# Kernel tuning notes

Measured on AMD Instinct MI355X. Metric: run time of the kernel, lower is better.

The kernel has to match this reference:

```python
import jax, jax.numpy as jnp
import numpy as np

# ---- constants hard-coded in the torch module ----
NEG_EPS = 1e-30          # eps used in log clamps
TAU = 0.35               # near-field temperature (getattr default)
K0 = 128                 # near-field band width
C_EMBD, N_HEADS, RANK = 768, 12, 32
B, T = 1, 2048


def _lin(k, fin, fout):
    lim = 1.0 / np.sqrt(fin)
    return jax.random.uniform(k, (fin, fout), jnp.float32, -lim, lim)


def _bias(k, fin, fout):
    lim = 1.0 / np.sqrt(fin)
    return jax.random.uniform(k, (fout,), jnp.float32, -lim, lim)


def setup_inputs() -> dict:
    key = jax.random.key(0)
    ks = jax.random.split(key, 24)
    C, H, R = C_EMBD, N_HEADS, RANK
    return {
        "x": jax.random.normal(ks[0], (B, T, C), jnp.float32),
        "Wq_w": _lin(ks[1], C, C), "Wq_b": _bias(ks[2], C, C),
        "Wk_w": _lin(ks[3], C, C), "Wk_b": _bias(ks[4], C, C),
        "Wv_w": _lin(ks[5], C, C), "Wv_b": _bias(ks[6], C, C),
        "Wo_w": _lin(ks[7], C, C), "Wo_b": _bias(ks[8], C, C),
        "Pq_w": _lin(ks[9], C, R),
        "Pk_w": _lin(ks[10], C, R),
        "Pv_w": _lin(ks[11], C, R),
        "up_w": _lin(ks[12], R, C),
        "gate_u": jax.random.normal(ks[13], (H, C // H), jnp.float32),
        "gate_b": jnp.zeros((H,), jnp.float32),
        "Wz_w": _lin(ks[14], 4 * C, C), "Wz_b": _bias(ks[15], 4 * C, C),
    }


def reference(x, Wq_w, Wq_b, Wk_w, Wk_b, Wv_w, Wv_b, Wo_w, Wo_b,
              Pq_w, Pk_w, Pv_w, up_w, gate_u, gate_b, Wz_w, Wz_b):
    Bx, Tx, C = x.shape
    H = gate_u.shape[0]
    D = C // H
    R = Pq_w.shape[1]
    k0 = min(K0, Tx - 1)
    kernel = k0 + 1
    b_scalar = -np.log(max(Tx, 1)).astype(np.float32) if hasattr(np.log(1.0), 'astype') else -np.log(max(Tx, 1))
    b_scalar = jnp.float32(-np.log(max(Tx, 1)))

    # 0) projections + heads
    Q = x @ Wq_w + Wq_b
    K = x @ Wk_w + Wk_b
    V = x @ Wv_w + Wv_b
    heads = lambda z: z.reshape(Bx, Tx, H, D).transpose(0, 2, 1, 3)  # (B,H,T,D)
    Qh, Kh, Vh = heads(Q), heads(K), heads(V)

    idx = jnp.arange(Tx)
    causal = idx[None, :] <= idx[:, None]                  # (T,T)
    band = causal & ((idx[:, None] - idx[None, :]) <= k0)  # banded causal

    # 1) low-rank EA + sigmoid + LASER seed
    Qr, Kr, Vr = Q @ Pq_w, K @ Pk_w, V @ Pv_w              # (B,T,R)
    S = (Qr @ Kr.transpose(0, 2, 1)) * (1.0 / np.sqrt(R))  # (B,T,T)
    # masked logits were -1e9 -> sigmoid == 0 exactly in fp32
    A_seed = jnp.where(causal[None], jax.nn.sigmoid(S * S + b_scalar), 0.0)
    # running causal max over keys, per feature (== amax of causally masked keys)
    m_seed = jax.lax.cummax(Vr, axis=1)                    # (B,T,R)
    Yr = jnp.einsum('bij,bjr->bir', A_seed, jnp.exp(Vr)) * jnp.exp(-m_seed)
    H0 = (jnp.log(jnp.maximum(Yr, NEG_EPS)) + m_seed) @ up_w  # (B,T,C)

    # 2a) near-field banded causal attention (cos^2 / tau, sigmoid, LASER)
    l2n = lambda z: z / jnp.maximum(jnp.linalg.norm(z, axis=-1, keepdims=True), 1e-12)
    cos = jnp.einsum('bhid,bhjd->bhij', l2n(Qh), l2n(Kh))  # (B,H,T,T)
    A_near = jnp.where(band[None, None], jax.nn.sigmoid(cos * cos / TAU + b_scalar), 0.0)
    # sliding-window (width kernel, past-only) max of V per feature
    m_near = jax.lax.reduce_window(
        Vh, -jnp.inf, jax.lax.max,
        window_dimensions=(1, 1, kernel, 1), window_strides=(1, 1, 1, 1),
        padding=[(0, 0), (0, 0), (kernel - 1, 0), (0, 0)])   # (B,H,T,D)
    V_exp = jnp.exp(Vh - m_near)
    Y_near = jnp.einsum('bhij,bhjd->bhid', A_near, V_exp)
    H_near = jnp.log(jnp.maximum(Y_near, NEG_EPS)) + m_near

    # 2b) far-field hierarchical levels: source truncates mid-loop; the
    # accumulator H_far_total_h is initialized to zeros -> contributes zero.
    Ht_h = H_near                                          # (B,H,T,D)

    # 3) head-wise sigmoid gating
    g = jax.nn.sigmoid(jnp.einsum('bhtd,hd->bht', Ht_h, gate_u) + gate_b[None, :, None])
    Ht_h = Ht_h * g[..., None]
    Htilde = Ht_h.transpose(0, 2, 1, 3).reshape(Bx, Tx, C)

    # 4) GRU blend (Wz consumes 4*C features)
    z = jax.nn.sigmoid(jnp.concatenate([x, H0, Htilde, H0 * Htilde], axis=-1) @ Wz_w + Wz_b)
    H_out = (1.0 - z) * H0 + z * Htilde
    return H_out @ Wo_w + Wo_b
```

## Files before the change

kernel.cpp:

```cpp
#include <hip/hip_runtime.h>
#include <math.h>

static constexpr float B_SCALAR    = -7.6246189861593985f;
static constexpr float INV_TAU     = 2.8571428571428571f;
static constexpr float INV_SQRT_R  = 0.17677669529663687f;

typedef __attribute__((ext_vector_type(8))) short bf16x8;
typedef __attribute__((ext_vector_type(4))) float f32x4;

__device__ __forceinline__ unsigned short f2b(float f) {
    union { float f; unsigned int u; } v; v.f = f;
    unsigned int r = v.u + 0x7fffu + ((v.u >> 16) & 1u);
    return (unsigned short)(r >> 16);
}

typedef const __attribute__((address_space(1))) unsigned int* gp1_t;
typedef __attribute__((address_space(3))) unsigned int* lp3_t;
__device__ __forceinline__ void gload16(const unsigned short* g, unsigned short* l) {
    __builtin_amdgcn_global_load_lds((gp1_t)g, (lp3_t)l, 16, 0, 0);
}

__device__ __forceinline__ bf16x8 frag128(const unsigned short* base, int row, int elem) {
    int byte = (row * 128 + elem * 2) ^ ((row & 7) << 4);
    return *(const bf16x8*)((const char*)base + byte);
}
__device__ __forceinline__ bf16x8 frag384(const unsigned short* base, int row, int elem) {
    int byte = (row * 384 + elem * 2) ^ ((row & 7) << 4);
    return *(const bf16x8*)((const char*)base + byte);
}

template<int MODE, int KZ>
__global__ __launch_bounds__(256) void gemm_mfma(
    const unsigned short* __restrict__ A0, const unsigned short* __restrict__ A1,
    const unsigned short* __restrict__ A2, const unsigned short* __restrict__ A3,
    const unsigned short* __restrict__ Bt, const float* __restrict__ bias,
    float* __restrict__ outf, unsigned short* __restrict__ outb,
    float* __restrict__ pbuf, int K, int ldo)
{
    __shared__ unsigned short As[2][128*64];
    __shared__ unsigned short Bs[2][128*64];
    const int tid = threadIdx.x;
    const int lane = tid & 63, wid = tid >> 6;
    const int wr = wid >> 1, wc = wid & 1;
    const int fr = lane & 15, fq = lane >> 4;
    const int n0 = blockIdx.x * 128, m0 = blockIdx.y * 128;
    const int kz = blockIdx.z;
    const int kslice = K / KZ;
    const int kbase = kz * kslice;
    const int nt = kslice / 64;

    f32x4 acc[4][4];
#pragma unroll
    for (int mi = 0; mi < 4; ++mi)
#pragma unroll
        for (int ni = 0; ni < 4; ++ni) acc[mi][ni] = (f32x4){0.f, 0.f, 0.f, 0.f};

    auto stage = [&](int buf, int k0) {
        const unsigned short* Ap;
        int k0l, ldA;
        if (MODE == 1) {
            int p = k0 / 768;
            Ap = (p == 0) ? A0 : (p == 1) ? A1 : (p == 2) ? A2 : A3;
            k0l = k0 - p * 768; ldA = 768;
        } else { Ap = A0; k0l = k0; ldA = K; }
#pragma unroll
        for (int i = 0; i < 4; ++i) {
            int cb = i * 256 + wid * 64;
            int c  = cb + lane;
            int r = c >> 3;
            int col = ((c & 7) ^ (r & 7)) * 8;
            gload16(Ap + (size_t)(m0 + r) * ldA + k0l + col, &As[buf][cb * 8]);
            gload16(Bt + (size_t)(n0 + r) * K   + k0  + col, &Bs[buf][cb * 8]);
        }
    };

    stage(0, kbase);
    asm volatile("s_waitcnt vmcnt(0)" ::: "memory");
    __builtin_amdgcn_s_barrier();
    __builtin_amdgcn_sched_barrier(0);

    int cur = 0;
    for (int t = 0; t < nt; ++t) {
        if (t + 1 < nt) stage(cur ^ 1, kbase + (t + 1) * 64);
#pragma unroll
        for (int kk = 0; kk < 64; kk += 32) {
            bf16x8 af[4], bfr[4];
#pragma unroll
            for (int mi = 0; mi < 4; ++mi)
                af[mi] = frag128(As[cur], wr*64 + mi*16 + fr, kk + fq*8);
#pragma unroll
            for (int ni = 0; ni < 4; ++ni)
                bfr[ni] = frag128(Bs[cur], wc*64 + ni*16 + fr, kk + fq*8);
#pragma unroll
            for (int mi = 0; mi < 4; ++mi)
#pragma unroll
                for (int ni = 0; ni < 4; ++ni)
                    acc[mi][ni] = __builtin_amdgcn_mfma_f32_16x16x32_bf16(
                        af[mi], bfr[ni], acc[mi][ni], 0, 0, 0);
        }
        asm volatile("s_waitcnt vmcnt(0)" ::: "memory");
        __builtin_amdgcn_s_barrier();
        __builtin_amdgcn_sched_barrier(0);
        cur ^= 1;
    }
#pragma unroll
    for (int mi = 0; mi < 4; ++mi)
#pragma unroll
        for (int ni = 0; ni < 4; ++ni)
#pragma unroll
            for (int v = 0; v < 4; ++v) {
                int m = m0 + wr*64 + mi*16 + fq*4 + v;
                int n = n0 + wc*64 + ni*16 + fr;
                float val = acc[mi][ni][v];
                if (KZ > 1) {
                    pbuf[((size_t)kz * 2048 + m) * 768 + n] = val;
                } else {
                    float vv = val + bias[n];
                    outf[(size_t)m * ldo + n] = vv;
                    if (MODE == 0) outb[(size_t)m * ldo + n] = f2b(vv);
                }
            }
}

__global__ __launch_bounds__(256) void wz_combine(
    const float* __restrict__ pbuf, const float* __restrict__ bz,
    const float* __restrict__ h0, const float* __restrict__ htl,
    unsigned short* __restrict__ outb)
{
    int i = blockIdx.x * 256 + threadIdx.x;
    if (i >= 2048*768/4) return;
    float4 s = *(const float4*)&pbuf[i*4];
    float4 p1 = *(const float4*)&pbuf[1536*1024 + i*4];
    float4 p2 = *(const float4*)&pbuf[2*1536*1024 + i*4];
    float4 p3 = *(const float4*)&pbuf[3*1536*1024 + i*4];
    s.x += p1.x + p2.x + p3.x; s.y += p1.y + p2.y + p3.y;
    s.z += p1.z + p2.z + p3.z; s.w += p1.w + p2.w + p3.w;
    float4 b = *(const float4*)&bz[(i % 192) * 4];
    float4 a = *(const float4*)&h0[i*4];
    float4 t = *(const float4*)&htl[i*4];
    float z0 = 1.f/(1.f+expf(-(s.x+b.x))), z1 = 1.f/(1.f+expf(-(s.y+b.y)));
    float z2 = 1.f/(1.f+expf(-(s.z+b.z))), z3 = 1.f/(1.f+expf(-(s.w+b.w)));
    outb[i*4+0] = f2b((1.f-z0)*a.x + z0*t.x);
    outb[i*4+1] = f2b((1.f-z1)*a.y + z1*t.y);
    outb[i*4+2] = f2b((1.f-z2)*a.z + z2*t.z);
    outb[i*4+3] = f2b((1.f-z3)*a.w + z3*t.w);
}

__global__ __launch_bounds__(256) void wo_combine(
    const float* __restrict__ pbuf, const float* __restrict__ bo,
    float* __restrict__ out)
{
    int i = blockIdx.x * 256 + threadIdx.x;
    if (i >= 2048*768/4) return;
    float4 s = *(const float4*)&pbuf[i*4];
    float4 p1 = *(const float4*)&pbuf[1536*1024 + i*4];
    float4 b = *(const float4*)&bo[(i % 192) * 4];
    float4 o;
    o.x = s.x + p1.x + b.x; o.y = s.y + p1.y + b.y;
    o.z = s.z + p1.z + b.z; o.w = s.w + p1.w + b.w;
    *(float4*)&out[i*4] = o;
}

__global__ __launch_bounds__(256) void cvt_bf16(const float* __restrict__ in,
                                                unsigned short* __restrict__ out, int n4)
{
    int i = blockIdx.x * 256 + threadIdx.x;
    if (i < n4) {
        float4 v = *(const float4*)&in[i * 4];
        out[i*4+0] = f2b(v.x); out[i*4+1] = f2b(v.y);
        out[i*4+2] = f2b(v.z); out[i*4+3] = f2b(v.w);
    }
}

__global__ __launch_bounds__(256) void transpose_w(const float* __restrict__ w,
                                                   unsigned short* __restrict__ wt,
                                                   int K, int N)
{
    __shared__ float tile[32][33];
    int kb = blockIdx.x * 32, nb = blockIdx.y * 32;
    int tx = threadIdx.x & 31, ty = threadIdx.x >> 5;
#pragma unroll
    for (int s = 0; s < 32; s += 8)
        tile[ty + s][tx] = w[(size_t)(kb + ty + s) * N + nb + tx];
    __syncthreads();
#pragma unroll
    for (int s = 0; s < 32; s += 8)
        wt[(size_t)(nb + ty + s) * K + kb + tx] = f2b(tile[tx][ty + s]);
}

__global__ void concat_bias(const float* __restrict__ bq, const float* __restrict__ bk,
                            const float* __restrict__ bv, float* __restrict__ o)
{
    int n = blockIdx.x * 256 + threadIdx.x;
    if (n < 2304) o[n] = (n < 768) ? bq[n] : (n < 1536) ? bk[n - 768] : bv[n - 1536];
}

__global__ __launch_bounds__(256) void build_gru_inputs(
    const float* __restrict__ h0, const float* __restrict__ hn,
    unsigned short* __restrict__ h0b, unsigned short* __restrict__ htlb,
    unsigned short* __restrict__ prodb, int n4)
{
    int i = blockIdx.x * 256 + threadIdx.x;
    if (i < n4) {
        float4 a = *(const float4*)&h0[i * 4];
        float4 b = *(const float4*)&hn[i * 4];
        h0b[i*4+0] = f2b(a.x); h0b[i*4+1] = f2b(a.y); h0b[i*4+2] = f2b(a.z); h0b[i*4+3] = f2b(a.w);
        htlb[i*4+0] = f2b(b.x); htlb[i*4+1] = f2b(b.y); htlb[i*4+2] = f2b(b.z); htlb[i*4+3] = f2b(b.w);
        prodb[i*4+0] = f2b(a.x*b.x); prodb[i*4+1] = f2b(a.y*b.y);
        prodb[i*4+2] = f2b(a.z*b.z); prodb[i*4+3] = f2b(a.w*b.w);
    }
}

__global__ __launch_bounds__(256) void lowrank_mfma(
    const unsigned short* __restrict__ qkvb, const unsigned short* __restrict__ pT,
    float* __restrict__ pbuf)
{
    __shared__ unsigned short As[2][128*64];
    __shared__ unsigned short Bs[2][32*64];
    const int tid = threadIdx.x, lane = tid & 63, wid = tid >> 6;
    const int fr = lane & 15, fq = lane >> 4;
    const int m0 = blockIdx.x * 128;
    const int sel = blockIdx.y, kz = blockIdx.z;
    const int kbase = kz * 192;

    f32x4 acc[2][2];
#pragma unroll
    for (int mi = 0; mi < 2; ++mi)
#pragma unroll
        for (int ni = 0; ni < 2; ++ni) acc[mi][ni] = (f32x4){0.f,0.f,0.f,0.f};

    auto stage = [&](int buf, int k0) {
#pragma unroll
        for (int i = 0; i < 4; ++i) {
            int cb = i * 256 + wid * 64, c = cb + lane;
            int r = c >> 3, col = ((c & 7) ^ (r & 7)) * 8;
            gload16(qkvb + (size_t)(m0 + r) * 2304 + sel*768 + k0 + col, &As[buf][cb * 8]);
        }
        {
            int cb = wid * 64, c = cb + lane;
            int r = c >> 3, col = ((c & 7) ^ (r & 7)) * 8;
            gload16(pT + (size_t)sel * 32*768 + (size_t)r * 768 + k0 + col, &Bs[buf][cb * 8]);
        }
    };

    stage(0, kbase);
    asm volatile("s_waitcnt vmcnt(0)" ::: "memory");
    __builtin_amdgcn_s_barrier();
    __builtin_amdgcn_sched_barrier(0);

    int cur = 0;
    for (int t = 0; t < 3; ++t) {
        if (t + 1 < 3) stage(cur ^ 1, kbase + (t + 1) * 64);
#pragma unroll
        for (int kk = 0; kk < 64; kk += 32) {
            bf16x8 a[2], b[2];
#pragma unroll
            for (int mi = 0; mi < 2; ++mi)
                a[mi] = frag128(As[cur], wid*32 + mi*16 + fr, kk + fq*8);
#pragma unroll
            for (int ni = 0; ni < 2; ++ni)
                b[ni] = frag128(Bs[cur], ni*16 + fr, kk + fq*8);
#pragma unroll
            for (int mi = 0; mi < 2; ++mi)
#pragma unroll
                for (int ni = 0; ni < 2; ++ni)
                    acc[mi][ni] = __builtin_amdgcn_mfma_f32_16x16x32_bf16(
                        a[mi], b[ni], acc[mi][ni], 0, 0, 0);
        }
        asm volatile("s_waitcnt vmcnt(0)" ::: "memory");
        __builtin_amdgcn_s_barrier();
        __builtin_amdgcn_sched_barrier(0);
        cur ^= 1;
    }
#pragma unroll
    for (int mi = 0; mi < 2; ++mi)
#pragma unroll
        for (int ni = 0; ni < 2; ++ni)
#pragma unroll
            for (int v = 0; v < 4; ++v) {
                int m = m0 + wid*32 + mi*16 + fq*4 + v;
                int n = ni*16 + fr;
                pbuf[((size_t)(kz*3 + sel) * 2048 + m) * 32 + n] = acc[mi][ni][v];
            }
}

__global__ __launch_bounds__(256) void lowrank_finish(
    const float* __restrict__ pbuf,
    unsigned short* __restrict__ qrb, unsigned short* __restrict__ krb,
    float* __restrict__ vr, unsigned short* __restrict__ evtb)
{
    int idx = blockIdx.x * 256 + threadIdx.x;
    int sel = idx >> 16, rem = idx & 65535;
    float s = pbuf[(size_t)(0*3 + sel)*65536 + rem]
            + pbuf[(size_t)(1*3 + sel)*65536 + rem]
            + pbuf[(size_t)(2*3 + sel)*65536 + rem]
            + pbuf[(size_t)(3*3 + sel)*65536 + rem];
    if (sel == 0)      qrb[rem] = f2b(s * INV_SQRT_R);
    else if (sel == 1) krb[rem] = f2b(s);
    else {
        int t = rem >> 5, r = rem & 31;
        vr[rem] = s;
        evtb[(size_t)r * 2048 + t] = f2b(expf(s));
    }
}

__global__ __launch_bounds__(256) void cummax_vr(const float* __restrict__ vr,
                                                 float* __restrict__ ms)
{
    __shared__ float part[256];
    int r = blockIdx.x, tid = threadIdx.x;
    int t0 = tid * 8;
    float v[8];
    float run = -INFINITY;
#pragma unroll
    for (int e = 0; e < 8; ++e) { run = fmaxf(run, vr[(t0+e)*32 + r]); v[e] = run; }
    part[tid] = run;
    __syncthreads();
    for (int off = 1; off < 256; off <<= 1) {
        float other = (tid >= off) ? part[tid - off] : -INFINITY;
        __syncthreads();
        part[tid] = fmaxf(part[tid], other);
        __syncthreads();
    }
    float excl = (tid > 0) ? part[tid - 1] : -INFINITY;
#pragma unroll
    for (int e = 0; e < 8; ++e) ms[(t0+e)*32 + r] = fmaxf(v[e], excl);
}

__global__ __launch_bounds__(256) void seed_mfma(
    const unsigned short* __restrict__ qrb, const unsigned short* __restrict__ krb,
    const unsigned short* __restrict__ evtb, float* __restrict__ partial)
{
    int it = blockIdx.x, jc = blockIdx.y;
    if (jc > it) return;
    const int i0 = it * 128, j0 = jc * 128;
    __shared__ unsigned short Qs[128*32];
    __shared__ unsigned short Ks[128*32];
    __shared__ unsigned short Es[32*128];
    __shared__ unsigned short Ps[128*128];
    const int tid = threadIdx.x, lane = tid & 63, wid = tid >> 6;
    const int fr = lane & 15, fq = lane >> 4;

#pragma unroll
    for (int s = 0; s < 2; ++s) {
        int cb = s * 256 + wid * 64;
        int c = cb + lane;
        int r = c >> 2, col = (c & 3) * 8;
        gload16(qrb + (size_t)(i0 + r) * 32 + col, &Qs[cb * 8]);
        gload16(krb + (size_t)(j0 + r) * 32 + col, &Ks[cb * 8]);
    }
#pragma unroll
    for (int s = 0; s < 2; ++s) {
        int c = s * 256 + tid;
        int rr = c >> 4, cc = c & 15;
        bf16x8 v = *(const bf16x8*)&evtb[(size_t)rr * 2048 + j0 + cc * 8];
        int byte = (rr * 256 + cc * 16) ^ ((rr & 7) << 4);
        *(bf16x8*)((char*)Es + byte) = v;
    }
    __syncthreads();

    const int wr = wid >> 1, wc = wid & 1;
    bf16x8 af[4], bk[4];
#pragma unroll
    for (int mi = 0; mi < 4; ++mi)
        af[mi] = *(const bf16x8*)&Qs[(wr*64 + mi*16 + fr)*32 + fq*8];
#pragma unroll
    for (int ni = 0; ni < 4; ++ni)
        bk[ni] = *(const bf16x8*)&Ks[(wc*64 + ni*16 + fr)*32 + fq*8];
#pragma unroll
    for (int mi = 0; mi < 4; ++mi)
#pragma unroll
        for (int ni = 0; ni < 4; ++ni) {
            f32x4 s4 = __builtin_amdgcn_mfma_f32_16x16x32_bf16(
                af[mi], bk[ni], (f32x4){0.f,0.f,0.f,0.f}, 0, 0, 0);
#pragma unroll
            for (int v = 0; v < 4; ++v) {
                int row = wr*64 + mi*16 + fq*4 + v;
                int col = wc*64 + ni*16 + fr;
                float a = 0.f;
                if (j0 + col <= i0 + row) {
                    float s = s4[v];
                    a = 1.f / (1.f + expf(-(s*s + B_SCALAR)));
                }
                int byte = (row * 256 + col * 2) ^ ((row & 7) << 4);
                *(unsigned short*)((char*)Ps + byte) = f2b(a);
            }
        }
    __syncthreads();

    f32x4 yacc[2][2];
#pragma unroll
    for (int mi = 0; mi < 2; ++mi)
#pragma unroll
        for (int nf = 0; nf < 2; ++nf) yacc[mi][nf] = (f32x4){0.f,0.f,0.f,0.f};
#pragma unroll
    for (int ks = 0; ks < 4; ++ks) {
        bf16x8 pa[2], eb[2];
#pragma unroll
        for (int mi = 0; mi < 2; ++mi) {
            int row = wid*32 + mi*16 + fr;
            int byte = (row * 256 + ks * 64 + fq * 16) ^ ((row & 7) << 4);
            pa[mi] = *(const bf16x8*)((const char*)Ps + byte);
        }
#pragma unroll
        for (int nf = 0; nf < 2; ++nf) {
            int rrow = nf*16 + fr;
            int byte = (rrow * 256 + ks * 64 + fq * 16) ^ ((rrow & 7) << 4);
            eb[nf] = *(const bf16x8*)((const char*)Es + byte);
        }
#pragma unroll
        for (int mi = 0; mi < 2; ++mi)
#pragma unroll
            for (int nf = 0; nf < 2; ++nf)
                yacc[mi][nf] = __builtin_amdgcn_mfma_f32_16x16x32_bf16(
                    pa[mi], eb[nf], yacc[mi][nf], 0, 0, 0);
    }
    float* pout = partial + ((size_t)(it*16 + jc) * 128) * 32;
#pragma unroll
    for (int mi = 0; mi < 2; ++mi)
#pragma unroll
        for (int nf = 0; nf < 2; ++nf)
#pragma unroll
            for (int v = 0; v < 4; ++v) {
                int row = wid*32 + mi*16 + fq*4 + v;
                int col = nf*16 + fr;
                pout[row*32 + col] = yacc[mi][nf][v];
            }
}

__global__ __launch_bounds__(256) void seed_finish(const float* __restrict__ partial,
                                                   const float* __restrict__ ms,
                                                   float* __restrict__ lr)
{
    int idx = blockIdx.x * 256 + threadIdx.x;
    int i = idx >> 5, r = idx & 31;
    int it = i >> 7, row = i & 127;
    float y = 0.f;
    for (int jjc = 0; jjc <= it; ++jjc)
        y += partial[(((size_t)(it*16 + jjc) * 128) + row) * 32 + r];
    float m = ms[idx];
    lr[idx] = logf(fmaxf(y * expf(-m), 1e-30f)) + m;
}

__global__ __launch_bounds__(256) void up_proj(const float* __restrict__ lr,
                                               const float* __restrict__ up,
                                               float* __restrict__ h0)
{
    __shared__ float ls[32];
    int t = blockIdx.x, tid = threadIdx.x;
    if (tid < 32) ls[tid] = lr[t*32 + tid];
    __syncthreads();
    for (int c = tid; c < 768; c += 256) {
        float acc = 0.f;
#pragma unroll
        for (int rr = 0; rr < 32; ++rr) acc = fmaf(ls[rr], up[rr*768 + c], acc);
        h0[t*768 + c] = acc;
    }
}

__global__ void head_norms_write(const float* __restrict__ qkv,
                                 unsigned short* __restrict__ qhatb,
                                 unsigned short* __restrict__ khatb)
{
    int t = blockIdx.x, tid = threadIdx.x;
    int h = tid >> 6, d = tid & 63;
    float q = qkv[t*2304 + h*64 + d];
    float k = qkv[t*2304 + 768 + h*64 + d];
    float sq = q*q, sk = k*k;
#pragma unroll
    for (int off = 32; off; off >>= 1) { sq += __shfl_xor(sq, off); sk += __shfl_xor(sk, off); }
    float iq = 1.f / fmaxf(sqrtf(sq), 1e-12f);
    float ik = 1.f / fmaxf(sqrtf(sk), 1e-12f);
    qhatb[(size_t)t*768 + h*64 + d] = f2b(q * iq);
    khatb[(size_t)t*768 + h*64 + d] = f2b(k * ik);
}

__global__ __launch_bounds__(256) void slide_max(const float* __restrict__ qkv,
                                                 float* __restrict__ mnear,
                                                 unsigned short* __restrict__ vexptb)
{
    __shared__ float vs[192][64];
    int c0 = blockIdx.x * 64, t0 = blockIdx.y * 64;
    int tid = threadIdx.x;
#pragma unroll
    for (int s = 0; s < 12; ++s) {
        int idx = tid + s * 256;
        int rr = idx >> 4, c4 = (idx & 15) * 4;
        int t = t0 - 128 + rr;
        float4 v4;
        if (t < 0) v4 = make_float4(-INFINITY, -INFINITY, -INFINITY, -INFINITY);
        else       v4 = *(const float4*)&qkv[t*2304 + 1536 + c0 + c4];
        *(float4*)&vs[rr][c4] = v4;
    }
    __syncthreads();
    int c = tid & 63, tg = tid >> 6;
    for (int u = 0; u < 16; ++u) {
        int tl = tg * 16 + u;
        float m = -INFINITY;
        for (int s = 0; s < 129; ++s) m = fmaxf(m, vs[tl + s][c]);
        float v = vs[tl + 128][c];
        int t = t0 + tl;
        mnear[(size_t)t*768 + c0 + c] = m;
        vexptb[(size_t)(c0 + c) * 2048 + t] = f2b(expf(v - m));
    }
}

__global__ __launch_bounds__(256) void near_fused(
    const unsigned short* __restrict__ qhatb, const unsigned short* __restrict__ khatb,
    const unsigned short* __restrict__ vexptb, const float* __restrict__ mnear,
    const float* __restrict__ gu, const float* __restrict__ gb,
    float* __restrict__ hn)
{
    __shared__ unsigned short Qs[64*64];
    __shared__ unsigned short KPs[192*64];
    __shared__ unsigned short Vst[64*192];
    const int it = blockIdx.x, hh = blockIdx.y;
    const int i0 = it * 64;
    const int tid = threadIdx.x, lane = tid & 63, wid = tid >> 6;
    const int fr = lane & 15, fq = lane >> 4;

#pragma unroll
    for (int i = 0; i < 2; ++i) {
        int cb = i * 256 + wid * 64, c = cb + lane;
        int r = c >> 3, col = ((c & 7) ^ (r & 7)) * 8;
        gload16(qhatb + (size_t)(i0 + r) * 768 + hh*64 + col, &Qs[cb * 8]);
    }
#pragma unroll
    for (int i = 0; i < 6; ++i) {
        int cb = i * 256 + wid * 64, c = cb + lane;
        int r = c >> 3, col = ((c & 7) ^ (r & 7)) * 8;
        int j = i0 - 128 + r; if (j < 0) j = 0;
        gload16(khatb + (size_t)j * 768 + hh*64 + col, &KPs[cb * 8]);
    }
#pragma unroll
    for (int i = 0; i < 6; ++i) {
        int cb = i * 256 + wid * 64, c = cb + lane;
        int d = c / 24, cc = c - d * 24;
        int ccp = (cc & 24) | ((cc & 7) ^ (d & 7));
        int t = i0 - 128 + ccp * 8; if (t < 0) t = 0;
        gload16(vexptb + (size_t)(hh*64 + d) * 2048 + t, &Vst[cb * 8]);
    }
    __syncthreads();

    f32x4 sacc[4][3];
#pragma unroll
    for (int mi = 0; mi < 4; ++mi)
#pragma unroll
        for (int ni = 0; ni < 3; ++ni) sacc[mi][ni] = (f32x4){0.f,0.f,0.f,0.f};
#pragma unroll
    for (int kt = 0; kt < 2; ++kt) {
        int kk = kt * 32;
        bf16x8 qa[4], kb[3];
#pragma unroll
        for (int mi = 0; mi < 4; ++mi)
            qa[mi] = frag128(Qs, mi*16 + fr, kk + fq*8);
#pragma unroll
        for (int ni = 0; ni < 3; ++ni)
            kb[ni] = frag128(KPs, wid*48 + ni*16 + fr, kk + fq*8);
#pragma unroll
        for (int mi = 0; mi < 4; ++mi)
#pragma unroll
            for (int ni = 0; ni < 3; ++ni)
                sacc[mi][ni] = __builtin_amdgcn_mfma_f32_16x16x32_bf16(
                    qa[mi], kb[ni], sacc[mi][ni], 0, 0, 0);
    }
    __syncthreads();

#pragma unroll
    for (int mi = 0; mi < 4; ++mi)
#pragma unroll
        for (int ni = 0; ni < 3; ++ni)
#pragma unroll
            for (int v = 0; v < 4; ++v) {
                int il = mi*16 + fq*4 + v;
                int jl = wid*48 + ni*16 + fr;
                float s = sacc[mi][ni][v];
                float a = 0.f;
                if (jl >= il && jl <= il + 128 && (i0 - 128 + jl) >= 0)
                    a = 1.f / (1.f + expf(-(s*s*INV_TAU + B_SCALAR)));
                int byte = (il * 384 + jl * 2) ^ ((il & 7) << 4);
                *(unsigned short*)((char*)KPs + byte) = f2b(a);
            }
    __syncthreads();

    f32x4 yacc[4];
#pragma unroll
    for (int nf = 0; nf < 4; ++nf) yacc[nf] = (f32x4){0.f,0.f,0.f,0.f};
#pragma unroll
    for (int ks = 0; ks < 6; ++ks) {
        int kk = ks * 32;
        bf16x8 pa = frag384(KPs, wid*16 + fr, kk + fq*8);
        bf16x8 vb[4];
#pragma unroll
        for (int nf = 0; nf < 4; ++nf)
            vb[nf] = frag384(Vst, nf*16 + fr, kk + fq*8);
#pragma unroll
        for (int nf = 0; nf < 4; ++nf)
            yacc[nf] = __builtin_amdgcn_mfma_f32_16x16x32_bf16(pa, vb[nf], yacc[nf], 0, 0, 0);
    }

    float hv[4][4];
    float sp[4] = {0.f, 0.f, 0.f, 0.f};
#pragma unroll
    for (int nf = 0; nf < 4; ++nf) {
        int d = nf*16 + fr;
        float guv = gu[hh*64 + d];
#pragma unroll
        for (int v = 0; v < 4; ++v) {
            int row = wid*16 + fq*4 + v;
            float y = yacc[nf][v];
            float h = logf(fmaxf(y, 1e-30f)) + mnear[(size_t)(i0 + row)*768 + hh*64 + d];
            hv[nf][v] = h;
            sp[v] = fmaf(h, guv, sp[v]);
        }
    }
#pragma unroll
    for (int off = 1; off < 16; off <<= 1) {
#pragma unroll
        for (int v = 0; v < 4; ++v) sp[v] += __shfl_xor(sp[v], off);
    }
    float gbh = gb[hh];
#pragma unroll
    for (int v = 0; v < 4; ++v) sp[v] = 1.f / (1.f + expf(-(sp[v] + gbh)));
#pragma unroll
    for (int nf = 0; nf < 4; ++nf)
#pragma unroll
        for (int v = 0; v < 4; ++v) {
            int row = wid*16 + fq*4 + v;
            int d = nf*16 + fr;
            hn[(size_t)(i0 + row)*768 + hh*64 + d] = hv[nf][v] * sp[v];
        }
}

extern "C" void kernel_launch(void* const* d_in, const int* in_sizes, int n_in,
                              void* d_out, int out_size, void* d_ws, size_t ws_size,
                              hipStream_t stream)
{
    const float* x  = (const float*)d_in[0];
    const float* wq = (const float*)d_in[1];  const float* bq = (const float*)d_in[2];
    const float* wk = (const float*)d_in[3];  const float* bk = (const float*)d_in[4];
    const float* wv = (const float*)d_in[5];  const float* bv = (const float*)d_in[6];
    const float* wo = (const float*)d_in[7];  const float* bo = (const float*)d_in[8];
    const float* pq = (const float*)d_in[9];  const float* pk = (const float*)d_in[10];
    const float* pv = (const float*)d_in[11];
    const float* up = (const float*)d_in[12];
    const float* gu = (const float*)d_in[13]; const float* gb = (const float*)d_in[14];
    const float* wz = (const float*)d_in[15]; const float* bz = (const float*)d_in[16];
    float* out = (float*)d_out;

    float* w = (float*)d_ws;
    float* qkv  = w; w += 2048*2304;
    float* vr   = w; w += 2048*32;
    float* ms   = w; w += 2048*32;
    float* lr   = w; w += 2048*32;
    float* h0   = w; w += 2048*768;
    float* mnear= w; w += 2048*768;
    float* hn   = w; w += 2048*768;
    float* partial = w; w += 16*16*128*32;
    float* pgemm = w; w += 4*2048*768;
    float* plr   = w; w += 4*3*2048*32;
    float* bqkv = w; w += 2304;
    unsigned short* xb     = (unsigned short*)w; w += 2048*768/2;
    unsigned short* qkvb   = (unsigned short*)w; w += 2048*2304/2;
    unsigned short* wqkvT  = (unsigned short*)w; w += 2304*768/2;
    unsigned short* wzT    = (unsigned short*)w; w += 768*3072/2;
    unsigned short* woT    = (unsigned short*)w; w += 768*768/2;
    unsigned short* pT     = (unsigned short*)w; w += 3*32*768/2;
    unsigned short* h0b    = (unsigned short*)w; w += 2048*768/2;
    unsigned short* htlb   = (unsigned short*)w; w += 2048*768/2;
    unsigned short* prodb  = (unsigned short*)w; w += 2048*768/2;
    unsigned short* houtb  = (unsigned short*)w; w += 2048*768/2;
    unsigned short* qrb    = (unsigned short*)w; w += 2048*32/2;
    unsigned short* krb    = (unsigned short*)w; w += 2048*32/2;
    unsigned short* evtb   = (unsigned short*)w; w += 32*2048/2;
    unsigned short* qhatb  = (unsigned short*)w; w += 2048*768/2;
    unsigned short* khatb  = (unsigned short*)w; w += 2048*768/2;
    unsigned short* vexptb = (unsigned short*)w; w += 768*2048/2;

    cvt_bf16<<<1536, 256, 0, stream>>>(x, xb, 2048*768/4);
    transpose_w<<<dim3(24,24), 256, 0, stream>>>(wq, wqkvT,            768, 768);
    transpose_w<<<dim3(24,24), 256, 0, stream>>>(wk, wqkvT + 768*768,  768, 768);
    transpose_w<<<dim3(24,24), 256, 0, stream>>>(wv, wqkvT + 1536*768, 768, 768);
    transpose_w<<<dim3(96,24), 256, 0, stream>>>(wz, wzT, 3072, 768);
    transpose_w<<<dim3(24,24), 256, 0, stream>>>(wo, woT, 768, 768);
    transpose_w<<<dim3(24,1),  256, 0, stream>>>(pq, pT,            768, 32);
    transpose_w<<<dim3(24,1),  256, 0, stream>>>(pk, pT + 32*768,   768, 32);
    transpose_w<<<dim3(24,1),  256, 0, stream>>>(pv, pT + 2*32*768, 768, 32);
    concat_bias<<<9, 256, 0, stream>>>(bq, bk, bv, bqkv);

    gemm_mfma<0,1><<<dim3(18,16,1), 256, 0, stream>>>(xb, nullptr, nullptr, nullptr,
        wqkvT, bqkv, qkv, qkvb, nullptr, 768, 2304);

    lowrank_mfma<<<dim3(16,3,4), 256, 0, stream>>>(qkvb, pT, plr);
    lowrank_finish<<<768, 256, 0, stream>>>(plr, qrb, krb, vr, evtb);
    cummax_vr<<<32, 256, 0, stream>>>(vr, ms);
    seed_mfma<<<dim3(16,16), 256, 0, stream>>>(qrb, krb, evtb, partial);
    seed_finish<<<256, 256, 0, stream>>>(partial, ms, lr);
    up_proj<<<2048, 256, 0, stream>>>(lr, up, h0);

    head_norms_write<<<2048, 768, 0, stream>>>(qkv, qhatb, khatb);
    slide_max<<<dim3(12,32), 256, 0, stream>>>(qkv, mnear, vexptb);
    near_fused<<<dim3(32,12), 256, 0, stream>>>(qhatb, khatb, vexptb, mnear, gu, gb, hn);

    build_gru_inputs<<<1536, 256, 0, stream>>>(h0, hn, h0b, htlb, prodb, 2048*768/4);
    gemm_mfma<1,4><<<dim3(6,16,4), 256, 0, stream>>>(xb, h0b, htlb, prodb,
        wzT, nullptr, nullptr, nullptr, pgemm, 3072, 768);
    wz_combine<<<1536, 256, 0, stream>>>(pgemm, bz, h0, hn, houtb);
    gemm_mfma<2,2><<<dim3(6,16,2), 256, 0, stream>>>(houtb, nullptr, nullptr, nullptr,
        woT, nullptr, nullptr, nullptr, pgemm, 768, 768);
    wo_combine<<<1536, 256, 0, stream>>>(pgemm, bo, out);
}
```

Before: 180.9 us.

## Merge prep kernels, fuse seed/up-proj and GRU input casts, speed sliding max

The ten weight/input preparation launches are merged into one prep_all kernel that dispatches by block index. seed_finish is folded into up_proj, which now also writes the bf16 copy of h0. near_fused now writes the bf16 Htilde and H0*Htilde products, so the build_gru_inputs pass is gone. slide_max computes its 129-wide window max from a shared core range plus prefix and suffix maxima instead of a full scan per row. Together these remove several launches and the extra global memory round trips, at the cost of more branching and an extra h0 read inside near_fused.

New measurement: 148.2 us. 18.1% less time.

```diff
diff --git a/kernel.cpp b/kernel.cpp
--- a/kernel.cpp
+++ b/kernel.cpp
@@ -161,54 +161,58 @@
     *(float4*)&out[i*4] = o;
 }
 
-__global__ __launch_bounds__(256) void cvt_bf16(const float* __restrict__ in,
-                                                unsigned short* __restrict__ out, int n4)
-{
-    int i = blockIdx.x * 256 + threadIdx.x;
-    if (i < n4) {
-        float4 v = *(const float4*)&in[i * 4];
-        out[i*4+0] = f2b(v.x); out[i*4+1] = f2b(v.y);
-        out[i*4+2] = f2b(v.z); out[i*4+3] = f2b(v.w);
-    }
-}
-
-__global__ __launch_bounds__(256) void transpose_w(const float* __restrict__ w,
-                                                   unsigned short* __restrict__ wt,
-                                                   int K, int N)
+__global__ __launch_bounds__(256) void prep_all(
+    const float* __restrict__ x, unsigned short* __restrict__ xb,
+    const float* __restrict__ wq, const float* __restrict__ wk,
+    const float* __restrict__ wv, unsigned short* __restrict__ wqkvT,
+    const float* __restrict__ wz, unsigned short* __restrict__ wzT,
+    const float* __restrict__ wo, unsigned short* __restrict__ woT,
+    const float* __restrict__ pq, const float* __restrict__ pk,
+    const float* __restrict__ pv, unsigned short* __restrict__ pT,
+    const float* __restrict__ bq, const float* __restrict__ bk,
+    const float* __restrict__ bv, float* __restrict__ bqkv)
 {
     __shared__ float tile[32][33];
-    int kb = blockIdx.x * 32, nb = blockIdx.y * 32;
+    int b = blockIdx.x;
+    if (b < 1536) {
+        int i = b * 256 + threadIdx.x;
+        float4 v = *(const float4*)&x[i * 4];
+        xb[i*4+0] = f2b(v.x); xb[i*4+1] = f2b(v.y);
+        xb[i*4+2] = f2b(v.z); xb[i*4+3] = f2b(v.w);
+        return;
+    }
+    b -= 1536;
+    const float* src; unsigned short* dst; int K, N, tb;
+    if (b < 1728) {
+        int sel = b / 576;
+        src = (sel == 0) ? wq : (sel == 1) ? wk : wv;
+        dst = wqkvT + (size_t)sel * 768 * 768;
+        K = 768; N = 768; tb = b - sel * 576;
+    } else if (b < 4032) {
+        src = wz; dst = wzT; K = 3072; N = 768; tb = b - 1728;
+    } else if (b < 4608) {
+        src = wo; dst = woT; K = 768; N = 768; tb = b - 4032;
+    } else if (b < 4680) {
+        int sel = (b - 4608) / 24;
+        src = (sel == 0) ? pq : (sel == 1) ? pk : pv;
+        dst = pT + (size_t)sel * 32 * 768;
+        K = 768; N = 32; tb = (b - 4608) % 24;
+    } else {
+        int n = (b - 4680) * 256 + threadIdx.x;
+        if (n < 2304)
+            bqkv[n] = (n < 768) ? bq[n] : (n < 1536) ? bk[n - 768] : bv[n - 1536];
+        return;
+    }
+    int kt = K / 32;
+    int kb = (tb % kt) * 32, nb = (tb / kt) * 32;
     int tx = threadIdx.x & 31, ty = threadIdx.x >> 5;
 #pragma unroll
     for (int s = 0; s < 32; s += 8)
-        tile[ty + s][tx] = w[(size_t)(kb + ty + s) * N + nb + tx];
+        tile[ty + s][tx] = src[(size_t)(kb + ty + s) * N + nb + tx];
     __syncthreads();
 #pragma unroll
     for (int s = 0; s < 32; s += 8)
-        wt[(size_t)(nb + ty + s) * K + kb + tx] = f2b(tile[tx][ty + s]);
-}
-
-__global__ void concat_bias(const float* __restrict__ bq, const float* __restrict__ bk,
-                            const float* __restrict__ bv, float* __restrict__ o)
-{
-    int n = blockIdx.x * 256 + threadIdx.x;
-    if (n < 2304) o[n] = (n < 768) ? bq[n] : (n < 1536) ? bk[n - 768] : bv[n - 1536];
-}
-
-__global__ __launch_bounds__(256) void build_gru_inputs(
-    const float* __restrict__ h0, const float* __restrict__ hn,
-    unsigned short* __restrict__ h0b, unsigned short* __restrict__ htlb,
-    unsigned short* __restrict__ prodb, int n4)
-{
-    int i = blockIdx.x * 256 + threadIdx.x;
-    if (i < n4) {
-        float4 a = *(const float4*)&h0[i * 4];
-        float4 b = *(const float4*)&hn[i * 4];
-        h0b[i*4+0] = f2b(a.x); h0b[i*4+1] = f2b(a.y); h0b[i*4+2] = f2b(a.z); h0b[i*4+3] = f2b(a.w);
-        htlb[i*4+0] = f2b(b.x); htlb[i*4+1] = f2b(b.y); htlb[i*4+2] = f2b(b.z); htlb[i*4+3] = f2b(b.w);
-        prodb[i*4+0] = f2b(a.x*b.x); prodb[i*4+1] = f2b(a.y*b.y);
-        prodb[i*4+2] = f2b(a.z*b.z); prodb[i*4+3] = f2b(a.w*b.w);
-    }
+        dst[(size_t)(nb + ty + s) * K + kb + tx] = f2b(tile[tx][ty + s]);
 }
 
 __global__ __launch_bounds__(256) void lowrank_mfma(
@@ -428,33 +432,29 @@
             }
 }
 
-__global__ __launch_bounds__(256) void seed_finish(const float* __restrict__ partial,
-                                                   const float* __restrict__ ms,
-                                                   float* __restrict__ lr)
-{
-    int idx = blockIdx.x * 256 + threadIdx.x;
-    int i = idx >> 5, r = idx & 31;
-    int it = i >> 7, row = i & 127;
-    float y = 0.f;
-    for (int jjc = 0; jjc <= it; ++jjc)
-        y += partial[(((size_t)(it*16 + jjc) * 128) + row) * 32 + r];
-    float m = ms[idx];
-    lr[idx] = logf(fmaxf(y * expf(-m), 1e-30f)) + m;
-}
-
-__global__ __launch_bounds__(256) void up_proj(const float* __restrict__ lr,
-                                               const float* __restrict__ up,
-                                               float* __restrict__ h0)
+__global__ __launch_bounds__(256) void seed_up(
+    const float* __restrict__ partial, const float* __restrict__ ms,
+    const float* __restrict__ up, float* __restrict__ h0,
+    unsigned short* __restrict__ h0b)
 {
     __shared__ float ls[32];
     int t = blockIdx.x, tid = threadIdx.x;
-    if (tid < 32) ls[tid] = lr[t*32 + tid];
+    if (tid < 32) {
+        int r = tid;
+        int it = t >> 7, row = t & 127;
+        float y = 0.f;
+        for (int jjc = 0; jjc <= it; ++jjc)
+            y += partial[(((size_t)(it*16 + jjc) * 128) + row) * 32 + r];
+        float m = ms[t*32 + r];
+        ls[r] = logf(fmaxf(y * expf(-m), 1e-30f)) + m;
+    }
     __syncthreads();
     for (int c = tid; c < 768; c += 256) {
         float acc = 0.f;
 #pragma unroll
         for (int rr = 0; rr < 32; ++rr) acc = fmaf(ls[rr], up[rr*768 + c], acc);
-        h0[t*768 + c] = acc;
+        h0[(size_t)t*768 + c] = acc;
+        h0b[(size_t)t*768 + c] = f2b(acc);
     }
 }
 
@@ -494,10 +494,22 @@
     }
     __syncthreads();
     int c = tid & 63, tg = tid >> 6;
+    const int TG = tg * 16;
+    float core = -INFINITY;
+    for (int s = TG + 15; s <= TG + 128; ++s) core = fmaxf(core, vs[s][c]);
+    float head[16], tail[16];
+    head[15] = -INFINITY;
+    float hs = -INFINITY;
+#pragma unroll
+    for (int u = 14; u >= 0; --u) { hs = fmaxf(hs, vs[TG + u][c]); head[u] = hs; }
+    tail[0] = -INFINITY;
+    float ts = -INFINITY;
+#pragma unroll
+    for (int u = 1; u <= 15; ++u) { ts = fmaxf(ts, vs[TG + 128 + u][c]); tail[u] = ts; }
+#pragma unroll
     for (int u = 0; u < 16; ++u) {
-        int tl = tg * 16 + u;
-        float m = -INFINITY;
-        for (int s = 0; s < 129; ++s) m = fmaxf(m, vs[tl + s][c]);
+        int tl = TG + u;
+        float m = fmaxf(fmaxf(core, head[u]), tail[u]);
         float v = vs[tl + 128][c];
         int t = t0 + tl;
         mnear[(size_t)t*768 + c0 + c] = m;
@@ -509,7 +521,8 @@
     const unsigned short* __restrict__ qhatb, const unsigned short* __restrict__ khatb,
     const unsigned short* __restrict__ vexptb, const float* __restrict__ mnear,
     const float* __restrict__ gu, const float* __restrict__ gb,
-    float* __restrict__ hn)
+    const float* __restrict__ h0, float* __restrict__ hn,
+    unsigned short* __restrict__ htlb, unsigned short* __restrict__ prodb)
 {
     __shared__ unsigned short Qs[64*64];
     __shared__ unsigned short KPs[192*64];
@@ -628,7 +641,11 @@
         for (int v = 0; v < 4; ++v) {
             int row = wid*16 + fq*4 + v;
             int d = nf*16 + fr;
-            hn[(size_t)(i0 + row)*768 + hh*64 + d] = hv[nf][v] * sp[v];
+            size_t idx = (size_t)(i0 + row)*768 + hh*64 + d;
+            float htl = hv[nf][v] * sp[v];
+            hn[idx] = htl;
+            htlb[idx] = f2b(htl);
+            prodb[idx] = f2b(h0[idx] * htl);
         }
 }
 
@@ -652,7 +669,6 @@
     float* qkv  = w; w += 2048*2304;
     float* vr   = w; w += 2048*32;
     float* ms   = w; w += 2048*32;
-    float* lr   = w; w += 2048*32;
     float* h0   = w; w += 2048*768;
     float* mnear= w; w += 2048*768;
     float* hn   = w; w += 2048*768;
@@ -677,16 +693,8 @@
     unsigned short* khatb  = (unsigned short*)w; w += 2048*768/2;
     unsigned short* vexptb = (unsigned short*)w; w += 768*2048/2;
 
-    cvt_bf16<<<1536, 256, 0, stream>>>(x, xb, 2048*768/4);
-    transpose_w<<<dim3(24,24), 256, 0, stream>>>(wq, wqkvT,            768, 768);
-    transpose_w<<<dim3(24,24), 256, 0, stream>>>(wk, wqkvT + 768*768,  768, 768);
-    transpose_w<<<dim3(24,24), 256, 0, stream>>>(wv, wqkvT + 1536*768, 768, 768);
-    transpose_w<<<dim3(96,24), 256, 0, stream>>>(wz, wzT, 3072, 768);
-    transpose_w<<<dim3(24,24), 256, 0, stream>>>(wo, woT, 768, 768);
-    transpose_w<<<dim3(24,1),  256, 0, stream>>>(pq, pT,            768, 32);
-    transpose_w<<<dim3(24,1),  256, 0, stream>>>(pk, pT + 32*768,   768, 32);
-    transpose_w<<<dim3(24,1),  256, 0, stream>>>(pv, pT + 2*32*768, 768, 32);
-    concat_bias<<<9, 256, 0, stream>>>(bq, bk, bv, bqkv);
+    prep_all<<<6225, 256, 0, stream>>>(x, xb, wq, wk, wv, wqkvT, wz, wzT,
+                                       wo, woT, pq, pk, pv, pT, bq, bk, bv, bqkv);
 
     gemm_mfma<0,1><<<dim3(18,16,1), 256, 0, stream>>>(xb, nullptr, nullptr, nullptr,
         wqkvT, bqkv, qkv, qkvb, nullptr, 768, 2304);
@@ -695,14 +703,13 @@
     lowrank_finish<<<768, 256, 0, stream>>>(plr, qrb, krb, vr, evtb);
     cummax_vr<<<32, 256, 0, stream>>>(vr, ms);
     seed_mfma<<<dim3(16,16), 256, 0, stream>>>(qrb, krb, evtb, partial);
-    seed_finish<<<256, 256, 0, stream>>>(partial, ms, lr);
-    up_proj<<<2048, 256, 0, stream>>>(lr, up, h0);
+    seed_up<<<2048, 256, 0, stream>>>(partial, ms, up, h0, h0b);
 
     head_norms_write<<<2048, 768, 0, stream>>>(qkv, qhatb, khatb);
     slide_max<<<dim3(12,32), 256, 0, stream>>>(qkv, mnear, vexptb);
-    near_fused<<<dim3(32,12), 256, 0, stream>>>(qhatb, khatb, vexptb, mnear, gu, gb, hn);
-
-    build_gru_inputs<<<1536, 256, 0, stream>>>(h0, hn, h0b, htlb, prodb, 2048*768/4);
+    near_fused<<<dim3(32,12), 256, 0, stream>>>(qhatb, khatb, vexptb, mnear,
+                                                gu, gb, h0, hn, htlb, prodb);
+
     gemm_mfma<1,4><<<dim3(6,16,4), 256, 0, stream>>>(xb, h0b, htlb, prodb,
         wzT, nullptr, nullptr, nullptr, pgemm, 3072, 768);
     wz_combine<<<1536, 256, 0, stream>>>(pgemm, bz, h0, hn, houtb);
```
